# Kernel optimization log

Hardware: AMD Instinct MI355X
Metric: run time of the kernel (lower is better)

The kernel has to match this reference:

```python
import jax, jax.numpy as jnp
import numpy as np

DT = 1.0
TAU_MEM_INV = 0.05
V_LEAK = 0.0
V_TH = 1.0
ALPHA = 100.0  # norse SuperSpike surrogate slope


@jax.custom_vjp
def spike_fn(x):
    # heaviside forward, SuperSpike surrogate backward (norse default 'super')
    return (x > 0).astype(x.dtype)

def _spike_fwd(x):
    return spike_fn(x), x

def _spike_bwd(x, g):
    return (g / (ALPHA * jnp.abs(x) + 1.0) ** 2,)

spike_fn.defvjp(_spike_fwd, _spike_bwd)


def setup_inputs() -> dict:
    key = jax.random.key(0)
    ks = jax.random.split(key, 7)
    T, B = 100, 256
    sizes = [784, 64, 64, 10]
    inp = jax.random.normal(ks[0], (T, B, 1, sizes[0]), dtype=jnp.float32)
    out = {"inp": inp}
    for i in range(3):
        fan_in = sizes[i]
        out[f"W{i}"] = jax.random.normal(ks[1 + 2 * i], (sizes[i + 1], fan_in), dtype=jnp.float32) * (1.0 / np.sqrt(fan_in)).astype(np.float32)
        out[f"b{i}"] = jax.random.normal(ks[2 + 2 * i], (sizes[i + 1],), dtype=jnp.float32) * 0.01
    return out


def _snn_forward(inp, Ws, bs):
    x_seq = inp.squeeze(2)  # [T, B, 784]
    B = x_seq.shape[1]
    v0 = tuple(jnp.zeros((B, W.shape[0]), x_seq.dtype) for W in Ws)

    def step(vs, x):
        new_vs = []
        layer_sp = []
        for W, b, v in zip(Ws, bs, vs):
            i_cur = x @ W.T + b                                  # [B, out]
            v = v + DT * TAU_MEM_INV * (V_LEAK - v + i_cur)      # leaky integrate
            z = spike_fn(v - V_TH)                               # fire
            v = v - z * V_TH                                     # reset_subtract
            x = z
            new_vs.append(v)
            layer_sp.append(z.reshape(-1))                       # x.flatten() per layer
        return tuple(new_vs), (x, jnp.concatenate(layer_sp))

    _, (out_spikes, layer_spikes) = jax.lax.scan(step, v0, x_seq)
    # out_spikes: [T, B, 10]; layer_spikes flattened time-major like torch.cat(list)
    return out_spikes, layer_spikes.reshape(-1)


def reference(inp, W0, b0, W1, b1, W2, b2):
    return _snn_forward(inp, (W0, W1, W2), (b0, b1, b2))
```

## Files before the change

kernel.cpp:

```cpp
#include <hip/hip_runtime.h>

#define T_STEPS 100
#define BATCH 256
#define NIN 784
#define N0 64
#define N1 64
#define N2 10
#define CHUNK (BATCH*N0 + BATCH*N1 + BATCH*N2)
#define I0ELEMS (25600*64)
#define NCHP 28

typedef __attribute__((ext_vector_type(8))) short short8;
typedef __attribute__((ext_vector_type(4))) float f32x4;

__device__ inline short bf16_rne(float x) {
  unsigned u = __float_as_uint(x);
  unsigned h = (u + 0x7FFFu + ((u >> 16) & 1u)) >> 16;
  return (short)h;
}
__device__ inline float bf16_val(short h) {
  return __uint_as_float(((unsigned)(unsigned short)h) << 16);
}

__global__ __launch_bounds__(256) void prep_w0_pack(
    const float* __restrict__ W0, short* __restrict__ W0p) {
  int idx = blockIdx.x * 256 + threadIdx.x;
  if (idx >= NCHP * 3 * 4 * 64 * 8) return;
  int e  = idx & 7;
  int r1 = idx >> 3;
  int l  = r1 & 63;
  int r2 = r1 >> 6;
  int ct = r2 & 3;
  int r3 = r2 >> 2;
  int p  = r3 % 3;
  int c  = r3 / 3;
  int k   = c * 32 + (l >> 4) * 8 + e;
  int col = ct * 16 + (l & 15);
  float w = (k < NIN) ? W0[col * NIN + k] : 0.0f;
  short h0 = bf16_rne(w);
  float rr1 = w - bf16_val(h0);
  short h1 = bf16_rne(rr1);
  float rr2 = rr1 - bf16_val(h1);
  short h2 = bf16_rne(rr2);
  W0p[idx] = (p == 0) ? h0 : (p == 1) ? h1 : h2;
}

__global__ __launch_bounds__(256, 2) void gemm0_kernel(
    const float* __restrict__ X, const short* __restrict__ W0p,
    const float* __restrict__ b0, float* __restrict__ I0T) {
  __shared__ float red[4][32][68];

  const int tid = threadIdx.x;
  const int r0  = blockIdx.x * 32;
  const int wid = tid >> 6;
  const int l   = tid & 63;
  const int lr  = l & 15;
  const int lk  = l >> 4;

  const int kbeg = wid * 224;

  f32x4 acc[2][4];
#pragma unroll
  for (int rt = 0; rt < 2; ++rt)
#pragma unroll
    for (int ct = 0; ct < 4; ++ct) acc[rt][ct] = f32x4{0.f, 0.f, 0.f, 0.f};

  const float*  xr0 = X + (size_t)(r0 + lr) * NIN;
  const float*  xr1 = xr0 + 16 * NIN;
  const short8* wp8 = (const short8*)W0p;

#pragma unroll
  for (int c = 0; c < 7; ++c) {
    const int k0 = kbeg + c * 32 + lk * 8;
    const int g  = wid * 7 + c;

    float4 xa0, xb0, xa1, xb1;
    if (k0 < NIN) {
      xa0 = *(const float4*)(xr0 + k0);
      xb0 = *(const float4*)(xr0 + k0 + 4);
      xa1 = *(const float4*)(xr1 + k0);
      xb1 = *(const float4*)(xr1 + k0 + 4);
    } else {
      xa0 = xb0 = xa1 = xb1 = float4{0.f, 0.f, 0.f, 0.f};
    }

    short8 cb[4][3];
#pragma unroll
    for (int ct = 0; ct < 4; ++ct) {
#pragma unroll
      for (int p = 0; p < 3; ++p)
        cb[ct][p] = wp8[(size_t)((g * 3 + p) * 4 + ct) * 64 + l];
    }

    short8 a0[3], a1[3];
    {
      float xs0[8] = {xa0.x, xa0.y, xa0.z, xa0.w, xb0.x, xb0.y, xb0.z, xb0.w};
      float xs1[8] = {xa1.x, xa1.y, xa1.z, xa1.w, xb1.x, xb1.y, xb1.z, xb1.w};
#pragma unroll
      for (int e = 0; e < 8; ++e) {
        float x  = xs0[e];
        short h0 = bf16_rne(x);   float rr1 = x - bf16_val(h0);
        short h1 = bf16_rne(rr1); float rr2 = rr1 - bf16_val(h1);
        a0[0][e] = h0; a0[1][e] = h1; a0[2][e] = bf16_rne(rr2);
        x  = xs1[e];
        h0 = bf16_rne(x);   rr1 = x - bf16_val(h0);
        h1 = bf16_rne(rr1); rr2 = rr1 - bf16_val(h1);
        a1[0][e] = h0; a1[1][e] = h1; a1[2][e] = bf16_rne(rr2);
      }
    }

#pragma unroll
    for (int ct = 0; ct < 4; ++ct) {
      {
        f32x4 a = acc[0][ct];
        a = __builtin_amdgcn_mfma_f32_16x16x32_bf16(a0[2], cb[ct][0], a, 0, 0, 0);
        a = __builtin_amdgcn_mfma_f32_16x16x32_bf16(a0[0], cb[ct][2], a, 0, 0, 0);
        a = __builtin_amdgcn_mfma_f32_16x16x32_bf16(a0[1], cb[ct][1], a, 0, 0, 0);
        a = __builtin_amdgcn_mfma_f32_16x16x32_bf16(a0[1], cb[ct][0], a, 0, 0, 0);
        a = __builtin_amdgcn_mfma_f32_16x16x32_bf16(a0[0], cb[ct][1], a, 0, 0, 0);
        a = __builtin_amdgcn_mfma_f32_16x16x32_bf16(a0[0], cb[ct][0], a, 0, 0, 0);
        acc[0][ct] = a;
      }
      {
        f32x4 a = acc[1][ct];
        a = __builtin_amdgcn_mfma_f32_16x16x32_bf16(a1[2], cb[ct][0], a, 0, 0, 0);
        a = __builtin_amdgcn_mfma_f32_16x16x32_bf16(a1[0], cb[ct][2], a, 0, 0, 0);
        a = __builtin_amdgcn_mfma_f32_16x16x32_bf16(a1[1], cb[ct][1], a, 0, 0, 0);
        a = __builtin_amdgcn_mfma_f32_16x16x32_bf16(a1[1], cb[ct][0], a, 0, 0, 0);
        a = __builtin_amdgcn_mfma_f32_16x16x32_bf16(a1[0], cb[ct][1], a, 0, 0, 0);
        a = __builtin_amdgcn_mfma_f32_16x16x32_bf16(a1[0], cb[ct][0], a, 0, 0, 0);
        acc[1][ct] = a;
      }
    }
  }

#pragma unroll
  for (int rt = 0; rt < 2; ++rt)
#pragma unroll
    for (int ct = 0; ct < 4; ++ct)
#pragma unroll
      for (int r = 0; r < 4; ++r)
        red[wid][rt * 16 + lk * 4 + r][ct * 16 + lr] = acc[rt][ct][r];
  __syncthreads();

  const int t0  = r0 >> 8;
  const int bb0 = r0 & 255;
  for (int idx = tid; idx < 32 * 16; idx += 256) {
    int row = idx >> 4, q = idx & 15;
    float4 v  = *(const float4*)&red[0][row][q * 4];
    float4 u1 = *(const float4*)&red[1][row][q * 4];
    float4 u2 = *(const float4*)&red[2][row][q * 4];
    float4 u3 = *(const float4*)&red[3][row][q * 4];
    v.x += u1.x; v.y += u1.y; v.z += u1.z; v.w += u1.w;
    v.x += u2.x; v.y += u2.y; v.z += u2.z; v.w += u2.w;
    v.x += u3.x; v.y += u3.y; v.z += u3.z; v.w += u3.w;
    float4 bv = ((const float4*)b0)[q];
    v.x += bv.x; v.y += bv.y; v.z += bv.z; v.w += bv.w;
    ((float4*)I0T)[((size_t)(bb0 + row) * T_STEPS + t0) * 16 + q] = v;
  }
}

__global__ __launch_bounds__(256) void fused_kernel(
    const float* __restrict__ I0T,
    const float* __restrict__ W1, const float* __restrict__ b1,
    const float* __restrict__ W2, const float* __restrict__ b2,
    float* __restrict__ out) {
  __shared__ float bufA[112][68];
  __shared__ float sW1t[64][68];
  __shared__ float sW2[N2][68];
  __shared__ float sI2[T_STEPS][N2];

  const int b   = blockIdx.x;
  const int tid = threadIdx.x;
  const int j   = tid & 63;
  const int tq  = tid >> 6;
  float* outSpk = out;
  float* laySpk = out + T_STEPS * BATCH * N2;

  {
    const float4* src = (const float4*)I0T + (size_t)b * (T_STEPS * 16);
    for (int idx = tid; idx < T_STEPS * 16; idx += 256) {
      float4 v = src[idx];
      int t = idx >> 4, j4 = idx & 15;
      *(float4*)&bufA[t][j4 * 4] = v;
    }
  }
  __syncthreads();

  if (tq == 0) {
    float v = 0.0f;
#pragma unroll
    for (int g = 0; g < 4; ++g) {
      float ic[25];
#pragma unroll
      for (int i = 0; i < 25; ++i) ic[i] = bufA[g * 25 + i][j];
#pragma unroll
      for (int i = 0; i < 25; ++i) {
        v = v + 0.05f * ((0.0f - v) + ic[i]);
        float z = (v > 1.0f) ? 1.0f : 0.0f;
        v -= z;
        ic[i] = z;
      }
#pragma unroll
      for (int i = 0; i < 25; ++i) bufA[g * 25 + i][j] = ic[i];
    }
  } else {
    for (int idx = tid - 64; idx < 64 * 16; idx += 192) {
      int i = idx >> 4, jv = idx & 15;
      float4 wv = *(const float4*)(W1 + (size_t)i * 64 + jv * 4);
      sW1t[jv * 4 + 0][i] = wv.x;
      sW1t[jv * 4 + 1][i] = wv.y;
      sW1t[jv * 4 + 2][i] = wv.z;
      sW1t[jv * 4 + 3][i] = wv.w;
    }
    for (int idx = tid - 64; idx < N2 * 16; idx += 192) {
      int o = idx >> 4, jv = idx & 15;
      *(float4*)&sW2[o][jv * 4] = *(const float4*)(W2 + (size_t)o * 64 + jv * 4);
    }
  }
  __syncthreads();

  for (int idx = tid; idx < T_STEPS * 16; idx += 256) {
    int t = idx >> 4, jv = idx & 15;
    *(float4*)(laySpk + (size_t)t * CHUNK + b * 64 + jv * 4) =
        *(const float4*)&bufA[t][jv * 4];
  }

  const int iq = tid & 15;
  const int ts = tid >> 4;
  float g1[4][7];
  {
    float4 bias = *(const float4*)(b1 + iq * 4);
#pragma unroll
    for (int tt = 0; tt < 7; ++tt) {
      g1[0][tt] = bias.x; g1[1][tt] = bias.y; g1[2][tt] = bias.z; g1[3][tt] = bias.w;
    }
#pragma unroll
    for (int jq = 0; jq < 16; ++jq) {
      float4 zv4[7];
#pragma unroll
      for (int tt = 0; tt < 7; ++tt)
        zv4[tt] = *(const float4*)&bufA[ts * 7 + tt][jq * 4];
      float4 w4[4];
#pragma unroll
      for (int e = 0; e < 4; ++e)
        w4[e] = *(const float4*)&sW1t[jq * 4 + e][iq * 4];
#pragma unroll
      for (int e = 0; e < 4; ++e) {
#pragma unroll
        for (int tt = 0; tt < 7; ++tt) {
          float zv = ((const float*)&zv4[tt])[e];
          g1[0][tt] = fmaf(zv, w4[e].x, g1[0][tt]);
          g1[1][tt] = fmaf(zv, w4[e].y, g1[1][tt]);
          g1[2][tt] = fmaf(zv, w4[e].z, g1[2][tt]);
          g1[3][tt] = fmaf(zv, w4[e].w, g1[3][tt]);
        }
      }
    }
  }
  __syncthreads();
#pragma unroll
  for (int tt = 0; tt < 7; ++tt) {
    float4 o = {g1[0][tt], g1[1][tt], g1[2][tt], g1[3][tt]};
    *(float4*)&bufA[ts * 7 + tt][iq * 4] = o;
  }
  __syncthreads();

  if (tq == 0) {
    float v = 0.0f;
#pragma unroll
    for (int g = 0; g < 4; ++g) {
      float ic[25];
#pragma unroll
      for (int i = 0; i < 25; ++i) ic[i] = bufA[g * 25 + i][j];
#pragma unroll
      for (int i = 0; i < 25; ++i) {
        v = v + 0.05f * ((0.0f - v) + ic[i]);
        float z = (v > 1.0f) ? 1.0f : 0.0f;
        v -= z;
        ic[i] = z;
      }
#pragma unroll
      for (int i = 0; i < 25; ++i) bufA[g * 25 + i][j] = ic[i];
    }
  }
  __syncthreads();

  for (int idx = tid; idx < T_STEPS * 16; idx += 256) {
    int t = idx >> 4, jv = idx & 15;
    *(float4*)(laySpk + (size_t)t * CHUNK + BATCH * N0 + b * 64 + jv * 4) =
        *(const float4*)&bufA[t][jv * 4];
  }

  for (int idx = tid; idx < T_STEPS * N2; idx += 256) {
    int t = idx / N2, o = idx % N2;
    float a = b2[o];
#pragma unroll
    for (int jq = 0; jq < 16; ++jq) {
      float4 z = *(const float4*)&bufA[t][jq * 4];
      float4 wv = *(const float4*)&sW2[o][jq * 4];
      a += z.x * wv.x;
      a += z.y * wv.y;
      a += z.z * wv.z;
      a += z.w * wv.w;
    }
    sI2[t][o] = a;
  }
  __syncthreads();

  if (tid < N2) {
    float v = 0.0f;
#pragma unroll
    for (int g = 0; g < 4; ++g) {
      float ic[25];
#pragma unroll
      for (int i = 0; i < 25; ++i) ic[i] = sI2[g * 25 + i][tid];
#pragma unroll
      for (int i = 0; i < 25; ++i) {
        v = v + 0.05f * ((0.0f - v) + ic[i]);
        float z = (v > 1.0f) ? 1.0f : 0.0f;
        v -= z;
        ic[i] = z;
      }
#pragma unroll
      for (int i = 0; i < 25; ++i) sI2[g * 25 + i][tid] = ic[i];
    }
  }
  __syncthreads();

  for (int idx = tid; idx < T_STEPS * N2; idx += 256) {
    int t = idx / N2, o = idx % N2;
    float z = sI2[t][o];
    outSpk[(size_t)t * (BATCH * N2) + b * N2 + o] = z;
    laySpk[(size_t)t * CHUNK + BATCH * (N0 + N1) + b * N2 + o] = z;
  }
}

extern "C" void kernel_launch(void* const* d_in, const int* in_sizes, int n_in,
                              void* d_out, int out_size, void* d_ws, size_t ws_size,
                              hipStream_t stream) {
  const float* inp = (const float*)d_in[0];
  const float* W0  = (const float*)d_in[1];
  const float* b0  = (const float*)d_in[2];
  const float* W1  = (const float*)d_in[3];
  const float* b1  = (const float*)d_in[4];
  const float* W2  = (const float*)d_in[5];
  const float* b2  = (const float*)d_in[6];

  float* I0T = (float*)d_ws;
  short* W0p = (short*)(I0T + I0ELEMS);

  prep_w0_pack<<<dim3(672), dim3(256), 0, stream>>>(W0, W0p);
  gemm0_kernel<<<dim3(800), dim3(256), 0, stream>>>(inp, W0p, b0, I0T);
  fused_kernel<<<dim3(BATCH), dim3(256), 0, stream>>>(I0T, W1, b1, W2, b2,
                                                      (float*)d_out);
}
```

Before: 53.69 us.

## Double-buffer X tiles into LDS via direct global-to-LDS loads in gemm0

Replaces the per-lane float4 global loads of the input activations in gemm0 with direct global_load_lds transfers into a per-wave double buffer in shared memory. The next K chunk is prefetched while the current one is converted and fed to the MFMAs, with explicit vmcnt waits. The aim is to hide global-load latency behind the 3-way bf16-split MFMA work. In exchange it adds LDS traffic, uses a hand-tuned waitcnt count that must match the number of outstanding loads, and adds a barrier before the reduction because the reduction buffer now aliases the staging buffers.

```diff
diff --git a/kernel.cpp b/kernel.cpp
--- a/kernel.cpp
+++ b/kernel.cpp
@@ -20,6 +20,12 @@
 }
 __device__ inline float bf16_val(short h) {
   return __uint_as_float(((unsigned)(unsigned short)h) << 16);
+}
+
+__device__ __forceinline__ void gl2lds16(const void* g, void* l) {
+  __builtin_amdgcn_global_load_lds(
+      (const __attribute__((address_space(1))) void*)g,
+      (__attribute__((address_space(3))) void*)l, 16, 0, 0);
 }
 
 __global__ __launch_bounds__(256) void prep_w0_pack(
@@ -48,7 +54,7 @@
 __global__ __launch_bounds__(256, 2) void gemm0_kernel(
     const float* __restrict__ X, const short* __restrict__ W0p,
     const float* __restrict__ b0, float* __restrict__ I0T) {
-  __shared__ float red[4][32][68];
+  __shared__ __align__(16) char smem[34816];
 
   const int tid = threadIdx.x;
   const int r0  = blockIdx.x * 32;
@@ -59,30 +65,42 @@
 
   const int kbeg = wid * 224;
 
+  char* Ab[2] = { smem + wid * 8192, smem + wid * 8192 + 4096 };
+  float (*red)[32][68] = (float(*)[32][68])smem;
+
   f32x4 acc[2][4];
 #pragma unroll
   for (int rt = 0; rt < 2; ++rt)
 #pragma unroll
     for (int ct = 0; ct < 4; ++ct) acc[rt][ct] = f32x4{0.f, 0.f, 0.f, 0.f};
 
-  const float*  xr0 = X + (size_t)(r0 + lr) * NIN;
-  const float*  xr1 = xr0 + 16 * NIN;
   const short8* wp8 = (const short8*)W0p;
+  const float4 z4 = {0.f, 0.f, 0.f, 0.f};
+
+  auto stageA = [&](int kb, char* buf) {
+    const int nv = max(0, min(4, (NIN - kb) / 8));
+#pragma unroll
+    for (int i = 0; i < 4; ++i) {
+      if (i < nv) {
+        const int g      = i * 64 + l;
+        const int row    = g & 31;
+        const int kgroup = g >> 5;
+        const float* src = X + (size_t)(r0 + row) * NIN + kb + kgroup * 4;
+        gl2lds16(src, buf + i * 1024);
+      } else {
+        *(float4*)(buf + (i * 64 + l) * 16) = z4;
+      }
+    }
+  };
+
+  stageA(kbeg, Ab[0]);
 
 #pragma unroll
   for (int c = 0; c < 7; ++c) {
-    const int k0 = kbeg + c * 32 + lk * 8;
-    const int g  = wid * 7 + c;
-
-    float4 xa0, xb0, xa1, xb1;
-    if (k0 < NIN) {
-      xa0 = *(const float4*)(xr0 + k0);
-      xb0 = *(const float4*)(xr0 + k0 + 4);
-      xa1 = *(const float4*)(xr1 + k0);
-      xb1 = *(const float4*)(xr1 + k0 + 4);
-    } else {
-      xa0 = xb0 = xa1 = xb1 = float4{0.f, 0.f, 0.f, 0.f};
-    }
+    const int kb  = kbeg + c * 32;
+    const int g   = wid * 7 + c;
+    const bool more = (c + 1 < 7);
+    char* cur = Ab[c & 1];
 
     short8 cb[4][3];
 #pragma unroll
@@ -92,20 +110,29 @@
         cb[ct][p] = wp8[(size_t)((g * 3 + p) * 4 + ct) * 64 + l];
     }
 
+    if (more) stageA(kb + 32, Ab[(c + 1) & 1]);
+
+    if (more) {
+      asm volatile("s_waitcnt vmcnt(16)" ::: "memory");
+    } else {
+      asm volatile("s_waitcnt vmcnt(12)" ::: "memory");
+    }
+    __builtin_amdgcn_sched_barrier(0);
+
     short8 a0[3], a1[3];
-    {
-      float xs0[8] = {xa0.x, xa0.y, xa0.z, xa0.w, xb0.x, xb0.y, xb0.z, xb0.w};
-      float xs1[8] = {xa1.x, xa1.y, xa1.z, xa1.w, xb1.x, xb1.y, xb1.z, xb1.w};
+#pragma unroll
+    for (int rt = 0; rt < 2; ++rt) {
+      const int row = rt * 16 + lr;
+      float4 fa = *(const float4*)(cur + (2 * lk) * 512 + row * 16);
+      float4 fb = *(const float4*)(cur + (2 * lk + 1) * 512 + row * 16);
+      float xs[8] = {fa.x, fa.y, fa.z, fa.w, fb.x, fb.y, fb.z, fb.w};
+      short8* dst0 = (rt == 0) ? &a0[0] : &a1[0];
 #pragma unroll
       for (int e = 0; e < 8; ++e) {
-        float x  = xs0[e];
+        float x  = xs[e];
         short h0 = bf16_rne(x);   float rr1 = x - bf16_val(h0);
         short h1 = bf16_rne(rr1); float rr2 = rr1 - bf16_val(h1);
-        a0[0][e] = h0; a0[1][e] = h1; a0[2][e] = bf16_rne(rr2);
-        x  = xs1[e];
-        h0 = bf16_rne(x);   rr1 = x - bf16_val(h0);
-        h1 = bf16_rne(rr1); rr2 = rr1 - bf16_val(h1);
-        a1[0][e] = h0; a1[1][e] = h1; a1[2][e] = bf16_rne(rr2);
+        dst0[0][e] = h0; dst0[1][e] = h1; dst0[2][e] = bf16_rne(rr2);
       }
     }
 
@@ -134,6 +161,7 @@
     }
   }
 
+  __syncthreads();
 #pragma unroll
   for (int rt = 0; rt < 2; ++rt)
 #pragma unroll
```

After: 58.71 us. 9.4% more time.
